# Kernel tuning notes

Measured on AMD Instinct MI355X. Metric: run time of the kernel, lower is better.

The kernel has to match this reference:

```python
import jax, jax.numpy as jnp
import numpy as np

NUM_LAYERS = 4
NUM_FOLDS = 512
FOLD_DIM = 64
ARITY = 2
BATCH = 2048
NUM_OUTPUTS = 8


def setup_inputs() -> dict:
    key = jax.random.key(0)
    k0, k1, k2, k3 = jax.random.split(key, 4)
    in_graph = jax.random.normal(k0, (BATCH, NUM_FOLDS, FOLD_DIM), dtype=jnp.float32)
    # per-layer folded dense weights, scaled for stability of repeated products
    weights = jax.random.normal(k1, (NUM_LAYERS, NUM_FOLDS, FOLD_DIM, FOLD_DIM), dtype=jnp.float32) / np.sqrt(FOLD_DIM)
    # address-book fold gather indices: for each layer, each output fold gathers ARITY input folds
    fold_idx = jax.random.randint(k2, (NUM_LAYERS, NUM_FOLDS, ARITY), 0, NUM_FOLDS)
    # final address-book entry: 1-D output fold index tensor
    out_idx = jax.random.randint(k3, (NUM_OUTPUTS,), 0, NUM_FOLDS)
    return {"in_graph": in_graph, "weights": weights, "fold_idx": fold_idx, "out_idx": out_idx}


def reference(in_graph, weights, fold_idx, out_idx):
    # DAG interpreter: for each entry, gather folds of prior module outputs
    # (AddressBook.in_fold_idx), combine (product layer), run folded submodule
    # (per-fold dense), then final entry gathers outputs via out_fold_idx.
    def step(x, layer):
        W, idx = layer                      # W: [F,K,K], idx: [F,ARITY]
        gathered = x[:, idx, :]             # [B,F,ARITY,K] irregular gather
        h = jnp.prod(gathered, axis=2)      # [B,F,K] Hadamard product layer
        y = jnp.einsum('bfk,fkj->bfj', h, W)  # folded dense sum layer
        return y, None

    x, _ = jax.lax.scan(step, in_graph, (weights, fold_idx))
    return x[:, out_idx, :]                 # [B, NUM_OUTPUTS, K]
```

## Files before the change

kernel.cpp:

```cpp
#include <hip/hip_runtime.h>

#define BATCH 2048
#define NF 512
#define FD 64
#define BT 16
#define SLOTF (16 * 17 * 4)

__global__ __launch_bounds__(512) void fused_dag_kernel(
    const float* __restrict__ in_graph,
    const float* __restrict__ weights,
    const int* __restrict__ fold_idx,
    const int* __restrict__ out_idx,
    float* __restrict__ out) {
  __shared__ float bufA[8 * SLOTF];
  __shared__ float bufB[4 * SLOTF];
  __shared__ int T[32];

  const int o    = blockIdx.x & 7;
  const int tile = blockIdx.x >> 3;
  const int B0   = tile * BT;
  const int t    = threadIdx.x;

  if (t == 0) {
    int f4 = out_idx[o];
    T[0] = f4;
    T[1] = fold_idx[(3 * NF + f4) * 2 + 0];
    T[2] = fold_idx[(3 * NF + f4) * 2 + 1];
    #pragma unroll
    for (int i = 0; i < 2; ++i) {
      int f = T[1 + i];
      T[3 + 2 * i]     = fold_idx[(2 * NF + f) * 2 + 0];
      T[3 + 2 * i + 1] = fold_idx[(2 * NF + f) * 2 + 1];
    }
    #pragma unroll
    for (int i = 0; i < 4; ++i) {
      int f = T[3 + i];
      T[7 + 2 * i]     = fold_idx[(1 * NF + f) * 2 + 0];
      T[7 + 2 * i + 1] = fold_idx[(1 * NF + f) * 2 + 1];
    }
    #pragma unroll
    for (int i = 0; i < 8; ++i) {
      int f = T[7 + i];
      T[15 + 2 * i]     = fold_idx[(0 * NF + f) * 2 + 0];
      T[15 + 2 * i + 1] = fold_idx[(0 * NF + f) * 2 + 1];
    }
  }
  __syncthreads();

  const int w  = t >> 6;
  const int l  = t & 63;
  const int tx = l & 15;
  const int ty = l >> 4;

  {
    const int node = w;
    float* slot = bufA + node * SLOTF;
    const int f0 = T[15 + 2 * node];
    const int f1 = T[16 + 2 * node];
    #pragma unroll
    for (int r = 0; r < 4; ++r) {
      const int b = ty * 4 + r;
      const float* row = in_graph + (size_t)(B0 + b) * NF * FD + tx * 4;
      float4 a = *(const float4*)(row + f0 * FD);
      float4 c = *(const float4*)(row + f1 * FD);
      float4 h;
      h.x = a.x * c.x; h.y = a.y * c.y; h.z = a.z * c.z; h.w = a.w * c.w;
      *(float4*)(slot + (tx * 17 + b) * 4) = h;
    }
    const float* W = weights + (size_t)(0 * NF + T[7 + node]) * (FD * FD);
    float4 acc[4];
    #pragma unroll
    for (int r = 0; r < 4; ++r) acc[r] = make_float4(0.f, 0.f, 0.f, 0.f);
    #pragma unroll 2
    for (int kq = 0; kq < 16; ++kq) {
      const float* Wk = W + kq * 4 * FD + tx * 4;
      float4 w0 = *(const float4*)(Wk);
      float4 w1 = *(const float4*)(Wk + FD);
      float4 w2 = *(const float4*)(Wk + 2 * FD);
      float4 w3 = *(const float4*)(Wk + 3 * FD);
      #pragma unroll
      for (int r = 0; r < 4; ++r) {
        float4 h = *(const float4*)(slot + (kq * 17 + 4 * r + ty) * 4);
        acc[r].x = fmaf(h.x, w0.x, acc[r].x); acc[r].y = fmaf(h.x, w0.y, acc[r].y);
        acc[r].z = fmaf(h.x, w0.z, acc[r].z); acc[r].w = fmaf(h.x, w0.w, acc[r].w);
        acc[r].x = fmaf(h.y, w1.x, acc[r].x); acc[r].y = fmaf(h.y, w1.y, acc[r].y);
        acc[r].z = fmaf(h.y, w1.z, acc[r].z); acc[r].w = fmaf(h.y, w1.w, acc[r].w);
        acc[r].x = fmaf(h.z, w2.x, acc[r].x); acc[r].y = fmaf(h.z, w2.y, acc[r].y);
        acc[r].z = fmaf(h.z, w2.z, acc[r].z); acc[r].w = fmaf(h.z, w2.w, acc[r].w);
        acc[r].x = fmaf(h.w, w3.x, acc[r].x); acc[r].y = fmaf(h.w, w3.y, acc[r].y);
        acc[r].z = fmaf(h.w, w3.z, acc[r].z); acc[r].w = fmaf(h.w, w3.w, acc[r].w);
      }
    }
    #pragma unroll
    for (int r = 0; r < 4; ++r)
      *(float4*)(slot + (tx * 17 + 4 * r + ty) * 4) = acc[r];
  }
  __syncthreads();

  {
    const int node = w >> 1, half = w & 1;
    const float* P0 = bufA + (2 * node) * SLOTF;
    const float* P1 = bufA + (2 * node + 1) * SLOTF;
    const float* W = weights + (size_t)(1 * NF + T[3 + node]) * (FD * FD);
    float* slot = bufB + node * SLOTF;
    float4 acc[2];
    acc[0] = make_float4(0.f, 0.f, 0.f, 0.f);
    acc[1] = make_float4(0.f, 0.f, 0.f, 0.f);
    #pragma unroll 2
    for (int kq = 0; kq < 16; ++kq) {
      const float* Wk = W + kq * 4 * FD + tx * 4;
      float4 w0 = *(const float4*)(Wk);
      float4 w1 = *(const float4*)(Wk + FD);
      float4 w2 = *(const float4*)(Wk + 2 * FD);
      float4 w3 = *(const float4*)(Wk + 3 * FD);
      #pragma unroll
      for (int r = 0; r < 2; ++r) {
        const int b = half * 8 + 4 * r + ty;
        float4 pa = *(const float4*)(P0 + (kq * 17 + b) * 4);
        float4 pb = *(const float4*)(P1 + (kq * 17 + b) * 4);
        float4 h;
        h.x = pa.x * pb.x; h.y = pa.y * pb.y; h.z = pa.z * pb.z; h.w = pa.w * pb.w;
        acc[r].x = fmaf(h.x, w0.x, acc[r].x); acc[r].y = fmaf(h.x, w0.y, acc[r].y);
        acc[r].z = fmaf(h.x, w0.z, acc[r].z); acc[r].w = fmaf(h.x, w0.w, acc[r].w);
        acc[r].x = fmaf(h.y, w1.x, acc[r].x); acc[r].y = fmaf(h.y, w1.y, acc[r].y);
        acc[r].z = fmaf(h.y, w1.z, acc[r].z); acc[r].w = fmaf(h.y, w1.w, acc[r].w);
        acc[r].x = fmaf(h.z, w2.x, acc[r].x); acc[r].y = fmaf(h.z, w2.y, acc[r].y);
        acc[r].z = fmaf(h.z, w2.z, acc[r].z); acc[r].w = fmaf(h.z, w2.w, acc[r].w);
        acc[r].x = fmaf(h.w, w3.x, acc[r].x); acc[r].y = fmaf(h.w, w3.y, acc[r].y);
        acc[r].z = fmaf(h.w, w3.z, acc[r].z); acc[r].w = fmaf(h.w, w3.w, acc[r].w);
      }
    }
    #pragma unroll
    for (int r = 0; r < 2; ++r)
      *(float4*)(slot + (tx * 17 + half * 8 + 4 * r + ty) * 4) = acc[r];
  }
  __syncthreads();

  {
    const int node = w >> 2, q = w & 3;
    const float* P0 = bufB + (2 * node) * SLOTF;
    const float* P1 = bufB + (2 * node + 1) * SLOTF;
    const float* W = weights + (size_t)(2 * NF + T[1 + node]) * (FD * FD);
    float* slot = bufA + node * SLOTF;
    const int b = q * 4 + ty;
    float4 acc = make_float4(0.f, 0.f, 0.f, 0.f);
    #pragma unroll 2
    for (int kq = 0; kq < 16; ++kq) {
      const float* Wk = W + kq * 4 * FD + tx * 4;
      float4 w0 = *(const float4*)(Wk);
      float4 w1 = *(const float4*)(Wk + FD);
      float4 w2 = *(const float4*)(Wk + 2 * FD);
      float4 w3 = *(const float4*)(Wk + 3 * FD);
      float4 pa = *(const float4*)(P0 + (kq * 17 + b) * 4);
      float4 pb = *(const float4*)(P1 + (kq * 17 + b) * 4);
      float4 h;
      h.x = pa.x * pb.x; h.y = pa.y * pb.y; h.z = pa.z * pb.z; h.w = pa.w * pb.w;
      acc.x = fmaf(h.x, w0.x, acc.x); acc.y = fmaf(h.x, w0.y, acc.y);
      acc.z = fmaf(h.x, w0.z, acc.z); acc.w = fmaf(h.x, w0.w, acc.w);
      acc.x = fmaf(h.y, w1.x, acc.x); acc.y = fmaf(h.y, w1.y, acc.y);
      acc.z = fmaf(h.y, w1.z, acc.z); acc.w = fmaf(h.y, w1.w, acc.w);
      acc.x = fmaf(h.z, w2.x, acc.x); acc.y = fmaf(h.z, w2.y, acc.y);
      acc.z = fmaf(h.z, w2.z, acc.z); acc.w = fmaf(h.z, w2.w, acc.w);
      acc.x = fmaf(h.w, w3.x, acc.x); acc.y = fmaf(h.w, w3.y, acc.y);
      acc.z = fmaf(h.w, w3.z, acc.z); acc.w = fmaf(h.w, w3.w, acc.w);
    }
    *(float4*)(slot + (tx * 17 + b) * 4) = acc;
  }
  __syncthreads();

  if (w < 4) {
    const float* P0 = bufA + 0 * SLOTF;
    const float* P1 = bufA + 1 * SLOTF;
    const float* W = weights + (size_t)(3 * NF + T[0]) * (FD * FD);
    const int b = w * 4 + ty;
    float4 acc = make_float4(0.f, 0.f, 0.f, 0.f);
    #pragma unroll 2
    for (int kq = 0; kq < 16; ++kq) {
      const float* Wk = W + kq * 4 * FD + tx * 4;
      float4 w0 = *(const float4*)(Wk);
      float4 w1 = *(const float4*)(Wk + FD);
      float4 w2 = *(const float4*)(Wk + 2 * FD);
      float4 w3 = *(const float4*)(Wk + 3 * FD);
      float4 pa = *(const float4*)(P0 + (kq * 17 + b) * 4);
      float4 pb = *(const float4*)(P1 + (kq * 17 + b) * 4);
      float4 h;
      h.x = pa.x * pb.x; h.y = pa.y * pb.y; h.z = pa.z * pb.z; h.w = pa.w * pb.w;
      acc.x = fmaf(h.x, w0.x, acc.x); acc.y = fmaf(h.x, w0.y, acc.y);
      acc.z = fmaf(h.x, w0.z, acc.z); acc.w = fmaf(h.x, w0.w, acc.w);
      acc.x = fmaf(h.y, w1.x, acc.x); acc.y = fmaf(h.y, w1.y, acc.y);
      acc.z = fmaf(h.y, w1.z, acc.z); acc.w = fmaf(h.y, w1.w, acc.w);
      acc.x = fmaf(h.z, w2.x, acc.x); acc.y = fmaf(h.z, w2.y, acc.y);
      acc.z = fmaf(h.z, w2.z, acc.z); acc.w = fmaf(h.z, w2.w, acc.w);
      acc.x = fmaf(h.w, w3.x, acc.x); acc.y = fmaf(h.w, w3.y, acc.y);
      acc.z = fmaf(h.w, w3.z, acc.z); acc.w = fmaf(h.w, w3.w, acc.w);
    }
    *(float4*)(out + ((size_t)(B0 + b) * 8 + o) * FD + tx * 4) = acc;
  }
}

extern "C" void kernel_launch(void* const* d_in, const int* in_sizes, int n_in,
                              void* d_out, int out_size, void* d_ws, size_t ws_size,
                              hipStream_t stream) {
  const float* in_graph = (const float*)d_in[0];
  const float* weights  = (const float*)d_in[1];
  const int*   fold_idx = (const int*)d_in[2];
  const int*   out_idx  = (const int*)d_in[3];
  float* out = (float*)d_out;

  fused_dag_kernel<<<(BATCH / BT) * 8, 512, 0, stream>>>(
      in_graph, weights, fold_idx, out_idx, out);
}
```

Measured before the change: 376.5 us.

## Split fused DAG kernel into per-layer launches through workspace buffers

Replaces the single fused kernel, where each block walks the whole 15-node tree for one output and batch tile, with four per-layer launches. Each launch processes one tree node per 64-row batch tile and writes intermediates to workspace. This gives every layer uniform work per block and removes the idle waves in the later stages of the fused version. In exchange it adds launch overhead and global-memory round trips for intermediates. It falls back to the fused kernel when the workspace is too small.

```diff
diff --git a/kernel.cpp b/kernel.cpp
--- a/kernel.cpp
+++ b/kernel.cpp
@@ -3,9 +3,93 @@
 #define BATCH 2048
 #define NF 512
 #define FD 64
+#define SLOT (16 * 17 * 4)
+
+__global__ __launch_bounds__(256) void layer_kernel(
+    const float* __restrict__ parents,
+    const float* __restrict__ weights,
+    const int* __restrict__ fold_idx,
+    const int* __restrict__ out_idx,
+    float* __restrict__ dest,
+    const int layer,
+    const long pSA, const long pSB,
+    const long oSA, const long oSB) {
+  __shared__ float lds[4 * SLOT];
+
+  const int node = blockIdx.x >> 5;
+  const int tile = blockIdx.x & 31;
+  const int t  = threadIdx.x;
+  const int w  = t >> 6;
+  const int l  = t & 63;
+  const int tx = l & 15;
+  const int ty = l >> 4;
+  const int R0 = tile * 64 + w * 16;
+
+  int f = out_idx[node >> (3 - layer)];
+  #pragma unroll
+  for (int L = 3; L > layer; --L)
+    f = fold_idx[(L * NF + f) * 2 + ((node >> (L - 1 - layer)) & 1)];
+
+  long c0, c1;
+  if (layer == 0) {
+    c0 = fold_idx[f * 2 + 0];
+    c1 = fold_idx[f * 2 + 1];
+  } else {
+    c0 = 2 * node;
+    c1 = 2 * node + 1;
+  }
+
+  float* slot = lds + w * SLOT;
+
+  {
+    const float* p0 = parents + c0 * pSA + tx * 4;
+    const float* p1 = parents + c1 * pSA + tx * 4;
+    #pragma unroll
+    for (int r = 0; r < 4; ++r) {
+      const int b = 4 * r + ty;
+      const long row = (long)(R0 + b);
+      float4 a = *(const float4*)(p0 + row * pSB);
+      float4 c = *(const float4*)(p1 + row * pSB);
+      float4 h;
+      h.x = a.x * c.x; h.y = a.y * c.y; h.z = a.z * c.z; h.w = a.w * c.w;
+      *(float4*)(slot + (tx * 17 + b) * 4) = h;
+    }
+  }
+
+  const float* W = weights + ((size_t)layer * NF + f) * (FD * FD);
+  float4 acc[4];
+  #pragma unroll
+  for (int r = 0; r < 4; ++r) acc[r] = make_float4(0.f, 0.f, 0.f, 0.f);
+  #pragma unroll 2
+  for (int kq = 0; kq < 16; ++kq) {
+    const float* Wk = W + kq * 4 * FD + tx * 4;
+    float4 w0 = *(const float4*)(Wk);
+    float4 w1 = *(const float4*)(Wk + FD);
+    float4 w2 = *(const float4*)(Wk + 2 * FD);
+    float4 w3 = *(const float4*)(Wk + 3 * FD);
+    #pragma unroll
+    for (int r = 0; r < 4; ++r) {
+      float4 h = *(const float4*)(slot + (kq * 17 + 4 * r + ty) * 4);
+      acc[r].x = fmaf(h.x, w0.x, acc[r].x); acc[r].y = fmaf(h.x, w0.y, acc[r].y);
+      acc[r].z = fmaf(h.x, w0.z, acc[r].z); acc[r].w = fmaf(h.x, w0.w, acc[r].w);
+      acc[r].x = fmaf(h.y, w1.x, acc[r].x); acc[r].y = fmaf(h.y, w1.y, acc[r].y);
+      acc[r].z = fmaf(h.y, w1.z, acc[r].z); acc[r].w = fmaf(h.y, w1.w, acc[r].w);
+      acc[r].x = fmaf(h.z, w2.x, acc[r].x); acc[r].y = fmaf(h.z, w2.y, acc[r].y);
+      acc[r].z = fmaf(h.z, w2.z, acc[r].z); acc[r].w = fmaf(h.z, w2.w, acc[r].w);
+      acc[r].x = fmaf(h.w, w3.x, acc[r].x); acc[r].y = fmaf(h.w, w3.y, acc[r].y);
+      acc[r].z = fmaf(h.w, w3.z, acc[r].z); acc[r].w = fmaf(h.w, w3.w, acc[r].w);
+    }
+  }
+
+  #pragma unroll
+  for (int r = 0; r < 4; ++r) {
+    const long row = (long)(R0 + 4 * r + ty);
+    *(float4*)(dest + node * oSA + row * oSB + tx * 4) = acc[r];
+  }
+}
+
 #define BT 16
 #define SLOTF (16 * 17 * 4)
-
 __global__ __launch_bounds__(512) void fused_dag_kernel(
     const float* __restrict__ in_graph,
     const float* __restrict__ weights,
@@ -207,6 +291,23 @@
   const int*   out_idx  = (const int*)d_in[3];
   float* out = (float*)d_out;
 
-  fused_dag_kernel<<<(BATCH / BT) * 8, 512, 0, stream>>>(
-      in_graph, weights, fold_idx, out_idx, out);
+  const size_t nodeF = (size_t)BATCH * FD;
+  const size_t need  = (64 + 32) * nodeF * sizeof(float);
+
+  if (ws_size >= need) {
+    float* b0 = (float*)d_ws;
+    float* b1 = b0 + 64 * nodeF;
+    const long NB = (long)nodeF;
+    layer_kernel<<<64 * 32, 256, 0, stream>>>(in_graph, weights, fold_idx, out_idx,
+        b0, 0, (long)FD, (long)NF * FD, NB, (long)FD);
+    layer_kernel<<<32 * 32, 256, 0, stream>>>(b0, weights, fold_idx, out_idx,
+        b1, 1, NB, (long)FD, NB, (long)FD);
+    layer_kernel<<<16 * 32, 256, 0, stream>>>(b1, weights, fold_idx, out_idx,
+        b0, 2, NB, (long)FD, NB, (long)FD);
+    layer_kernel<<<8 * 32, 256, 0, stream>>>(b0, weights, fold_idx, out_idx,
+        out, 3, NB, (long)FD, (long)FD, (long)(8 * FD));
+  } else {
+    fused_dag_kernel<<<(BATCH / BT) * 8, 512, 0, stream>>>(
+        in_graph, weights, fold_idx, out_idx, out);
+  }
 }
```

After: 387.2 us. +2.8%, slower.

## Split fused DAG kernel into two kernels with workspace intermediate

Applied to the files above, without the earlier changes.

Replaces the single fused kernel, which evaluates the whole 4-level tree per output and batch tile, with two kernels. The first computes layers 0-1 for the 32 level-2 input nodes and writes them to a workspace buffer. The second computes layers 2-3 for the 8 outputs, using 32-row batch tiles and padded shared memory. This spreads each block's weight loads over more batch rows and gives smaller blocks, but adds a global-memory round trip and a second launch. The original kernel remains as a fallback when the workspace is too small.

```diff
diff --git a/kernel.cpp b/kernel.cpp
--- a/kernel.cpp
+++ b/kernel.cpp
@@ -3,9 +3,208 @@
 #define BATCH 2048
 #define NF 512
 #define FD 64
+#define PAD_B 33
+#define CSLOT (16 * PAD_B * 4)
+
+__device__ __forceinline__ void fma16(float4& acc, const float4 h,
+                                      const float4 w0, const float4 w1,
+                                      const float4 w2, const float4 w3) {
+  acc.x = fmaf(h.x, w0.x, acc.x); acc.y = fmaf(h.x, w0.y, acc.y);
+  acc.z = fmaf(h.x, w0.z, acc.z); acc.w = fmaf(h.x, w0.w, acc.w);
+  acc.x = fmaf(h.y, w1.x, acc.x); acc.y = fmaf(h.y, w1.y, acc.y);
+  acc.z = fmaf(h.y, w1.z, acc.z); acc.w = fmaf(h.y, w1.w, acc.w);
+  acc.x = fmaf(h.z, w2.x, acc.x); acc.y = fmaf(h.z, w2.y, acc.y);
+  acc.z = fmaf(h.z, w2.z, acc.z); acc.w = fmaf(h.z, w2.w, acc.w);
+  acc.x = fmaf(h.w, w3.x, acc.x); acc.y = fmaf(h.w, w3.y, acc.y);
+  acc.z = fmaf(h.w, w3.z, acc.z); acc.w = fmaf(h.w, w3.w, acc.w);
+}
+
+__global__ __launch_bounds__(256) void fused01_kernel(
+    const float* __restrict__ in_graph,
+    const float* __restrict__ weights,
+    const int* __restrict__ fold_idx,
+    const int* __restrict__ out_idx,
+    float* __restrict__ b1) {
+  __shared__ float cslot[2 * CSLOT];
+
+  const int n    = blockIdx.x >> 6;
+  const int tile = blockIdx.x & 63;
+  const int t  = threadIdx.x;
+  const int w  = t >> 6;
+  const int l  = t & 63;
+  const int tx = l & 15;
+  const int ty = l >> 4;
+
+  int f = out_idx[n >> 2];
+  f = fold_idx[(3 * NF + f) * 2 + ((n >> 1) & 1)];
+  const int f1 = fold_idx[(2 * NF + f) * 2 + (n & 1)];
+
+  {
+    const int c = w >> 1, q = w & 1;
+    const int f0 = fold_idx[(1 * NF + f1) * 2 + c];
+    const int g0 = fold_idx[f0 * 2 + 0];
+    const int g1 = fold_idx[f0 * 2 + 1];
+    float* slot = cslot + c * CSLOT + q * 64;
+    #pragma unroll
+    for (int r = 0; r < 4; ++r) {
+      const int b = 4 * r + ty;
+      const float* row =
+          in_graph + (size_t)(tile * 32 + q * 16 + b) * (NF * FD) + tx * 4;
+      float4 a  = *(const float4*)(row + g0 * FD);
+      float4 c2 = *(const float4*)(row + g1 * FD);
+      float4 h;
+      h.x = a.x * c2.x; h.y = a.y * c2.y; h.z = a.z * c2.z; h.w = a.w * c2.w;
+      *(float4*)(slot + (tx * PAD_B + b) * 4) = h;
+    }
+    const float* W = weights + (size_t)f0 * (FD * FD);
+    float4 acc[4];
+    #pragma unroll
+    for (int r = 0; r < 4; ++r) acc[r] = make_float4(0.f, 0.f, 0.f, 0.f);
+    #pragma unroll 2
+    for (int kq = 0; kq < 16; ++kq) {
+      const float* Wk = W + kq * 4 * FD + tx * 4;
+      float4 w0 = *(const float4*)(Wk);
+      float4 w1 = *(const float4*)(Wk + FD);
+      float4 w2 = *(const float4*)(Wk + 2 * FD);
+      float4 w3 = *(const float4*)(Wk + 3 * FD);
+      #pragma unroll
+      for (int r = 0; r < 4; ++r) {
+        float4 h = *(const float4*)(slot + (kq * PAD_B + 4 * r + ty) * 4);
+        fma16(acc[r], h, w0, w1, w2, w3);
+      }
+    }
+    #pragma unroll
+    for (int r = 0; r < 4; ++r)
+      *(float4*)(slot + (tx * PAD_B + 4 * r + ty) * 4) = acc[r];
+  }
+  __syncthreads();
+
+  {
+    const float* P0 = cslot;
+    const float* P1 = cslot + CSLOT;
+    const float* W = weights + (size_t)(1 * NF + f1) * (FD * FD);
+    float4 acc[2];
+    acc[0] = make_float4(0.f, 0.f, 0.f, 0.f);
+    acc[1] = make_float4(0.f, 0.f, 0.f, 0.f);
+    #pragma unroll 2
+    for (int kq = 0; kq < 16; ++kq) {
+      const float* Wk = W + kq * 4 * FD + tx * 4;
+      float4 w0 = *(const float4*)(Wk);
+      float4 w1 = *(const float4*)(Wk + FD);
+      float4 w2 = *(const float4*)(Wk + 2 * FD);
+      float4 w3 = *(const float4*)(Wk + 3 * FD);
+      #pragma unroll
+      for (int r = 0; r < 2; ++r) {
+        const int b = w * 8 + 4 * r + ty;
+        float4 pa = *(const float4*)(P0 + (kq * PAD_B + b) * 4);
+        float4 pb = *(const float4*)(P1 + (kq * PAD_B + b) * 4);
+        float4 h;
+        h.x = pa.x * pb.x; h.y = pa.y * pb.y; h.z = pa.z * pb.z; h.w = pa.w * pb.w;
+        fma16(acc[r], h, w0, w1, w2, w3);
+      }
+    }
+    #pragma unroll
+    for (int r = 0; r < 2; ++r) {
+      const int b = w * 8 + 4 * r + ty;
+      *(float4*)(b1 + (size_t)n * (BATCH * FD) +
+                 (size_t)(tile * 32 + b) * FD + tx * 4) = acc[r];
+    }
+  }
+}
+
+__global__ __launch_bounds__(256) void fused23_kernel(
+    const float* __restrict__ b1,
+    const float* __restrict__ weights,
+    const int* __restrict__ fold_idx,
+    const int* __restrict__ out_idx,
+    float* __restrict__ out) {
+  __shared__ float cslot[2 * CSLOT];
+
+  const int o    = blockIdx.x >> 6;
+  const int tile = blockIdx.x & 63;
+  const int t  = threadIdx.x;
+  const int w  = t >> 6;
+  const int l  = t & 63;
+  const int tx = l & 15;
+  const int ty = l >> 4;
+
+  const int froot = out_idx[o];
+  const long NB = (long)BATCH * FD;
+
+  {
+    const int c = w >> 1, q = w & 1;
+    const int m  = 2 * o + c;
+    const int f2 = fold_idx[(3 * NF + froot) * 2 + c];
+    float* slot = cslot + c * CSLOT + q * 64;
+    const float* p0 = b1 + (size_t)(2 * m) * NB + tx * 4;
+    const float* p1 = b1 + (size_t)(2 * m + 1) * NB + tx * 4;
+    #pragma unroll
+    for (int r = 0; r < 4; ++r) {
+      const int b = 4 * r + ty;
+      const size_t roff = (size_t)(tile * 32 + q * 16 + b) * FD;
+      float4 a  = *(const float4*)(p0 + roff);
+      float4 c2 = *(const float4*)(p1 + roff);
+      float4 h;
+      h.x = a.x * c2.x; h.y = a.y * c2.y; h.z = a.z * c2.z; h.w = a.w * c2.w;
+      *(float4*)(slot + (tx * PAD_B + b) * 4) = h;
+    }
+    const float* W = weights + (size_t)(2 * NF + f2) * (FD * FD);
+    float4 acc[4];
+    #pragma unroll
+    for (int r = 0; r < 4; ++r) acc[r] = make_float4(0.f, 0.f, 0.f, 0.f);
+    #pragma unroll 2
+    for (int kq = 0; kq < 16; ++kq) {
+      const float* Wk = W + kq * 4 * FD + tx * 4;
+      float4 w0 = *(const float4*)(Wk);
+      float4 w1 = *(const float4*)(Wk + FD);
+      float4 w2 = *(const float4*)(Wk + 2 * FD);
+      float4 w3 = *(const float4*)(Wk + 3 * FD);
+      #pragma unroll
+      for (int r = 0; r < 4; ++r) {
+        float4 h = *(const float4*)(slot + (kq * PAD_B + 4 * r + ty) * 4);
+        fma16(acc[r], h, w0, w1, w2, w3);
+      }
+    }
+    #pragma unroll
+    for (int r = 0; r < 4; ++r)
+      *(float4*)(slot + (tx * PAD_B + 4 * r + ty) * 4) = acc[r];
+  }
+  __syncthreads();
+
+  {
+    const float* P0 = cslot;
+    const float* P1 = cslot + CSLOT;
+    const float* W = weights + (size_t)(3 * NF + froot) * (FD * FD);
+    float4 acc[2];
+    acc[0] = make_float4(0.f, 0.f, 0.f, 0.f);
+    acc[1] = make_float4(0.f, 0.f, 0.f, 0.f);
+    #pragma unroll 2
+    for (int kq = 0; kq < 16; ++kq) {
+      const float* Wk = W + kq * 4 * FD + tx * 4;
+      float4 w0 = *(const float4*)(Wk);
+      float4 w1 = *(const float4*)(Wk + FD);
+      float4 w2 = *(const float4*)(Wk + 2 * FD);
+      float4 w3 = *(const float4*)(Wk + 3 * FD);
+      #pragma unroll
+      for (int r = 0; r < 2; ++r) {
+        const int b = w * 8 + 4 * r + ty;
+        float4 pa = *(const float4*)(P0 + (kq * PAD_B + b) * 4);
+        float4 pb = *(const float4*)(P1 + (kq * PAD_B + b) * 4);
+        float4 h;
+        h.x = pa.x * pb.x; h.y = pa.y * pb.y; h.z = pa.z * pb.z; h.w = pa.w * pb.w;
+        fma16(acc[r], h, w0, w1, w2, w3);
+      }
+    }
+    #pragma unroll
+    for (int r = 0; r < 2; ++r) {
+      const int b = w * 8 + 4 * r + ty;
+      *(float4*)(out + (size_t)(tile * 32 + b) * (8 * FD) + o * FD + tx * 4) = acc[r];
+    }
+  }
+}
+
 #define BT 16
 #define SLOTF (16 * 17 * 4)
-
 __global__ __launch_bounds__(512) void fused_dag_kernel(
     const float* __restrict__ in_graph,
     const float* __restrict__ weights,
@@ -81,14 +280,7 @@
       #pragma unroll
       for (int r = 0; r < 4; ++r) {
         float4 h = *(const float4*)(slot + (kq * 17 + 4 * r + ty) * 4);
-        acc[r].x = fmaf(h.x, w0.x, acc[r].x); acc[r].y = fmaf(h.x, w0.y, acc[r].y);
-        acc[r].z = fmaf(h.x, w0.z, acc[r].z); acc[r].w = fmaf(h.x, w0.w, acc[r].w);
-        acc[r].x = fmaf(h.y, w1.x, acc[r].x); acc[r].y = fmaf(h.y, w1.y, acc[r].y);
-        acc[r].z = fmaf(h.y, w1.z, acc[r].z); acc[r].w = fmaf(h.y, w1.w, acc[r].w);
-        acc[r].x = fmaf(h.z, w2.x, acc[r].x); acc[r].y = fmaf(h.z, w2.y, acc[r].y);
-        acc[r].z = fmaf(h.z, w2.z, acc[r].z); acc[r].w = fmaf(h.z, w2.w, acc[r].w);
-        acc[r].x = fmaf(h.w, w3.x, acc[r].x); acc[r].y = fmaf(h.w, w3.y, acc[r].y);
-        acc[r].z = fmaf(h.w, w3.z, acc[r].z); acc[r].w = fmaf(h.w, w3.w, acc[r].w);
+        fma16(acc[r], h, w0, w1, w2, w3);
       }
     }
     #pragma unroll
@@ -120,14 +312,7 @@
         float4 pb = *(const float4*)(P1 + (kq * 17 + b) * 4);
         float4 h;
         h.x = pa.x * pb.x; h.y = pa.y * pb.y; h.z = pa.z * pb.z; h.w = pa.w * pb.w;
-        acc[r].x = fmaf(h.x, w0.x, acc[r].x); acc[r].y = fmaf(h.x, w0.y, acc[r].y);
-        acc[r].z = fmaf(h.x, w0.z, acc[r].z); acc[r].w = fmaf(h.x, w0.w, acc[r].w);
-        acc[r].x = fmaf(h.y, w1.x, acc[r].x); acc[r].y = fmaf(h.y, w1.y, acc[r].y);
-        acc[r].z = fmaf(h.y, w1.z, acc[r].z); acc[r].w = fmaf(h.y, w1.w, acc[r].w);
-        acc[r].x = fmaf(h.z, w2.x, acc[r].x); acc[r].y = fmaf(h.z, w2.y, acc[r].y);
-        acc[r].z = fmaf(h.z, w2.z, acc[r].z); acc[r].w = fmaf(h.z, w2.w, acc[r].w);
-        acc[r].x = fmaf(h.w, w3.x, acc[r].x); acc[r].y = fmaf(h.w, w3.y, acc[r].y);
-        acc[r].z = fmaf(h.w, w3.z, acc[r].z); acc[r].w = fmaf(h.w, w3.w, acc[r].w);
+        fma16(acc[r], h, w0, w1, w2, w3);
       }
     }
     #pragma unroll
@@ -155,14 +340,7 @@
       float4 pb = *(const float4*)(P1 + (kq * 17 + b) * 4);
       float4 h;
       h.x = pa.x * pb.x; h.y = pa.y * pb.y; h.z = pa.z * pb.z; h.w = pa.w * pb.w;
-      acc.x = fmaf(h.x, w0.x, acc.x); acc.y = fmaf(h.x, w0.y, acc.y);
-      acc.z = fmaf(h.x, w0.z, acc.z); acc.w = fmaf(h.x, w0.w, acc.w);
-      acc.x = fmaf(h.y, w1.x, acc.x); acc.y = fmaf(h.y, w1.y, acc.y);
-      acc.z = fmaf(h.y, w1.z, acc.z); acc.w = fmaf(h.y, w1.w, acc.w);
-      acc.x = fmaf(h.z, w2.x, acc.x); acc.y = fmaf(h.z, w2.y, acc.y);
-      acc.z = fmaf(h.z, w2.z, acc.z); acc.w = fmaf(h.z, w2.w, acc.w);
-      acc.x = fmaf(h.w, w3.x, acc.x); acc.y = fmaf(h.w, w3.y, acc.y);
-      acc.z = fmaf(h.w, w3.z, acc.z); acc.w = fmaf(h.w, w3.w, acc.w);
+      fma16(acc, h, w0, w1, w2, w3);
     }
     *(float4*)(slot + (tx * 17 + b) * 4) = acc;
   }
@@ -185,14 +363,7 @@
       float4 pb = *(const float4*)(P1 + (kq * 17 + b) * 4);
       float4 h;
       h.x = pa.x * pb.x; h.y = pa.y * pb.y; h.z = pa.z * pb.z; h.w = pa.w * pb.w;
-      acc.x = fmaf(h.x, w0.x, acc.x); acc.y = fmaf(h.x, w0.y, acc.y);
-      acc.z = fmaf(h.x, w0.z, acc.z); acc.w = fmaf(h.x, w0.w, acc.w);
-      acc.x = fmaf(h.y, w1.x, acc.x); acc.y = fmaf(h.y, w1.y, acc.y);
-      acc.z = fmaf(h.y, w1.z, acc.z); acc.w = fmaf(h.y, w1.w, acc.w);
-      acc.x = fmaf(h.z, w2.x, acc.x); acc.y = fmaf(h.z, w2.y, acc.y);
-      acc.z = fmaf(h.z, w2.z, acc.z); acc.w = fmaf(h.z, w2.w, acc.w);
-      acc.x = fmaf(h.w, w3.x, acc.x); acc.y = fmaf(h.w, w3.y, acc.y);
-      acc.z = fmaf(h.w, w3.z, acc.z); acc.w = fmaf(h.w, w3.w, acc.w);
+      fma16(acc, h, w0, w1, w2, w3);
     }
     *(float4*)(out + ((size_t)(B0 + b) * 8 + o) * FD + tx * 4) = acc;
   }
@@ -207,6 +378,16 @@
   const int*   out_idx  = (const int*)d_in[3];
   float* out = (float*)d_out;
 
-  fused_dag_kernel<<<(BATCH / BT) * 8, 512, 0, stream>>>(
-      in_graph, weights, fold_idx, out_idx, out);
-}
+  const size_t need = 32ull * BATCH * FD * sizeof(float);
+
+  if (ws_size >= need) {
+    float* b1 = (float*)d_ws;
+    fused01_kernel<<<32 * 64, 256, 0, stream>>>(
+        in_graph, weights, fold_idx, out_idx, b1);
+    fused23_kernel<<<8 * 64, 256, 0, stream>>>(
+        b1, weights, fold_idx, out_idx, out);
+  } else {
+    fused_dag_kernel<<<(BATCH / BT) * 8, 512, 0, stream>>>(
+        in_graph, weights, fold_idx, out_idx, out);
+  }
+}
```

Measured after the change: 389.0 us. 1.03x slower.
